# Kernel optimization log

Measured on AMD Instinct MI355X. Metric: run time of the kernel, lower is better.

Reference implementation:

```python
import jax, jax.numpy as jnp
import numpy as np

# x: (B, num_units, in_channels, unit_size)
B, NUM_UNITS, IN_CH, UNIT = 64, 32, 256, 128


def setup_inputs() -> dict:
    key = jax.random.key(0)
    x = jax.random.normal(key, (B, NUM_UNITS, IN_CH, UNIT), dtype=jnp.float32)
    return {"x": x}


def _squash(s):
    # squash over dim 3 (unit_size), matching CapsuleLayer.squash
    mag_sq = jnp.sum(s * s, axis=3, keepdims=True)
    mag = jnp.sqrt(mag_sq)
    return mag_sq / (1.0 + mag_sq) * (s / (mag + 1e-5))


def reference(x):
    b, nu, ic, us = x.shape
    # torch .reshape (memory reinterpret), NOT a transpose -- keep identical semantics
    u_hat = x.reshape(b, ic, nu, us, 1)  # (B, in_ch, num_units, unit, 1)
    # routing logits start at zero; single iteration => softmax gives uniform 1/in_ch
    b_ij = jnp.zeros((1, ic, nu, 1), dtype=x.dtype)
    c_ij = jax.nn.softmax(b_ij, axis=1)[..., None]  # (1, in_ch, num_units, 1, 1)
    # weighted sum over in_channels
    s_j = jnp.sum(c_ij * u_hat, axis=1, keepdims=True)  # (B, 1, num_units, unit, 1)
    v_j = _squash(s_j)
    # with num_iterations == 1 the b_ij agreement update never affects the output
    return v_j.squeeze(1)  # (B, num_units, unit, 1)
```

## Files before the change

### kernel.cpp

```cpp
#include <hip/hip_runtime.h>


#define BATCH     64
#define NUM_UNITS 32
#define IN_CH     256
#define UNIT      128

__global__ __launch_bounds__(256) void capsule_squash_kernel(
    const float* __restrict__ x, float* __restrict__ out)
{
    const int blk = blockIdx.x;
    const int b   = blk >> 5;
    const int n   = blk & 31;
    const int t   = threadIdx.x;
    const int f4  = t & 31;
    const int sub = t >> 5;

    const float4* __restrict__ xb =
        reinterpret_cast<const float4*>(x)
        + (size_t)b * 262144u + (size_t)n * 32u + (size_t)f4;

    float4 acc = make_float4(0.f, 0.f, 0.f, 0.f);
    #pragma unroll
    for (int k = 0; k < 32; ++k) {
        const int i = sub + (k << 3);
        const float4 v = xb[(size_t)i * 1024u];
        acc.x += v.x; acc.y += v.y; acc.z += v.z; acc.w += v.w;
    }

    __shared__ float4 lds[8][32];
    lds[sub][f4] = acc;
    __syncthreads();

    if (t < 32) {
        float4 s = lds[0][t];
        #pragma unroll
        for (int j = 1; j < 8; ++j) {
            const float4 v = lds[j][t];
            s.x += v.x; s.y += v.y; s.z += v.z; s.w += v.w;
        }
        const float inv = 1.0f / (float)IN_CH;
        s.x *= inv; s.y *= inv; s.z *= inv; s.w *= inv;

        float psq = s.x*s.x + s.y*s.y + s.z*s.z + s.w*s.w;
        #pragma unroll
        for (int m = 1; m <= 16; m <<= 1)
            psq += __shfl_xor(psq, m);

        const float mag   = sqrtf(psq);
        const float scale = psq / (1.0f + psq) / (mag + 1e-5f);
        s.x *= scale; s.y *= scale; s.z *= scale; s.w *= scale;

        float4* o = reinterpret_cast<float4*>(out) + (size_t)blk * 32u + t;
        *o = s;
    }
}

extern "C" void kernel_launch(void* const* d_in, const int* in_sizes, int n_in,
                              void* d_out, int out_size, void* d_ws, size_t ws_size,
                              hipStream_t stream)
{
    const float* x = (const float*)d_in[0];
    float* out = (float*)d_out;
    capsule_squash_kernel<<<BATCH * NUM_UNITS, 256, 0, stream>>>(x, out);
}
```

Before: 347.5 us.

## Split reduction into contiguous-chunk partial sums plus separate squash kernel

Measured after the change: 357.2 us. +2.8%, slower.

```diff
diff --git a/kernel.cpp b/kernel.cpp
--- a/kernel.cpp
+++ b/kernel.cpp
@@ -1,57 +1,77 @@
 #include <hip/hip_runtime.h>
 
 
-#define BATCH     64
-#define NUM_UNITS 32
-#define IN_CH     256
-#define UNIT      128
+#define ADD4(a, v) do { (a).x += (v).x; (a).y += (v).y; (a).z += (v).z; (a).w += (v).w; } while (0)
 
-__global__ __launch_bounds__(256) void capsule_squash_kernel(
-    const float* __restrict__ x, float* __restrict__ out)
+__global__ __launch_bounds__(256) void caps_partial_kernel(
+    const float* __restrict__ x, float* __restrict__ ws)
+{
+    const int blk = blockIdx.x;
+    const int b   = blk >> 4;
+    const int c   = blk & 15;
+    const int t   = threadIdx.x;
+
+    const float4* __restrict__ p =
+        reinterpret_cast<const float4*>(x) + ((size_t)b << 18) + ((size_t)c << 14) + t;
+
+    float4 a0 = make_float4(0.f,0.f,0.f,0.f);
+    float4 a1 = a0, a2 = a0, a3 = a0;
+
+    #pragma unroll 4
+    for (int k2 = 0; k2 < 16; ++k2) {
+        const float4* q = p + ((size_t)k2 << 10);
+        const float4 v0 = q[0];
+        const float4 v1 = q[256];
+        const float4 v2 = q[512];
+        const float4 v3 = q[768];
+        ADD4(a0, v0); ADD4(a1, v1); ADD4(a2, v2); ADD4(a3, v3);
+    }
+
+    float4* __restrict__ w = reinterpret_cast<float4*>(ws) + ((size_t)blk << 10) + t;
+    w[0]   = a0;
+    w[256] = a1;
+    w[512] = a2;
+    w[768] = a3;
+}
+
+__global__ __launch_bounds__(64) void caps_squash_kernel(
+    const float* __restrict__ ws, float* __restrict__ out)
 {
     const int blk = blockIdx.x;
     const int b   = blk >> 5;
     const int n   = blk & 31;
-    const int t   = threadIdx.x;
-    const int f4  = t & 31;
-    const int sub = t >> 5;
+    const int l   = threadIdx.x;
+    const int col = l & 31;
+    const int h   = l >> 5;
 
-    const float4* __restrict__ xb =
-        reinterpret_cast<const float4*>(x)
-        + (size_t)b * 262144u + (size_t)n * 32u + (size_t)f4;
+    const float4* __restrict__ w =
+        reinterpret_cast<const float4*>(ws) + ((size_t)b << 14) + (n << 5) + col;
 
-    float4 acc = make_float4(0.f, 0.f, 0.f, 0.f);
+    float4 s = make_float4(0.f,0.f,0.f,0.f);
     #pragma unroll
-    for (int k = 0; k < 32; ++k) {
-        const int i = sub + (k << 3);
-        const float4 v = xb[(size_t)i * 1024u];
-        acc.x += v.x; acc.y += v.y; acc.z += v.z; acc.w += v.w;
+    for (int j = 0; j < 8; ++j) {
+        const float4 v = w[(size_t)(h + (j << 1)) << 10];
+        ADD4(s, v);
     }
+    s.x += __shfl_xor(s.x, 32);
+    s.y += __shfl_xor(s.y, 32);
+    s.z += __shfl_xor(s.z, 32);
+    s.w += __shfl_xor(s.w, 32);
 
-    __shared__ float4 lds[8][32];
-    lds[sub][f4] = acc;
-    __syncthreads();
+    const float inv = 1.0f / 256.0f;
+    s.x *= inv; s.y *= inv; s.z *= inv; s.w *= inv;
 
-    if (t < 32) {
-        float4 s = lds[0][t];
-        #pragma unroll
-        for (int j = 1; j < 8; ++j) {
-            const float4 v = lds[j][t];
-            s.x += v.x; s.y += v.y; s.z += v.z; s.w += v.w;
-        }
-        const float inv = 1.0f / (float)IN_CH;
-        s.x *= inv; s.y *= inv; s.z *= inv; s.w *= inv;
+    float psq = s.x*s.x + s.y*s.y + s.z*s.z + s.w*s.w;
+    #pragma unroll
+    for (int m = 1; m <= 16; m <<= 1)
+        psq += __shfl_xor(psq, m);
 
-        float psq = s.x*s.x + s.y*s.y + s.z*s.z + s.w*s.w;
-        #pragma unroll
-        for (int m = 1; m <= 16; m <<= 1)
-            psq += __shfl_xor(psq, m);
+    const float mag   = sqrtf(psq);
+    const float scale = psq / (1.0f + psq) / (mag + 1e-5f);
+    s.x *= scale; s.y *= scale; s.z *= scale; s.w *= scale;
 
-        const float mag   = sqrtf(psq);
-        const float scale = psq / (1.0f + psq) / (mag + 1e-5f);
-        s.x *= scale; s.y *= scale; s.z *= scale; s.w *= scale;
-
-        float4* o = reinterpret_cast<float4*>(out) + (size_t)blk * 32u + t;
+    if (l < 32) {
+        float4* o = reinterpret_cast<float4*>(out) + ((size_t)blk << 5) + col;
         *o = s;
     }
 }
@@ -61,6 +81,8 @@
                               hipStream_t stream)
 {
     const float* x = (const float*)d_in[0];
+    float* ws  = (float*)d_ws;
     float* out = (float*)d_out;
-    capsule_squash_kernel<<<BATCH * NUM_UNITS, 256, 0, stream>>>(x, out);
+    caps_partial_kernel<<<64 * 16, 256, 0, stream>>>(x, ws);
+    caps_squash_kernel <<<64 * 32,  64, 0, stream>>>(ws, out);
 }
```
